# Performance work log

Measured on AMD Instinct MI355X. Metric: run time of the kernel, lower is better.

Reference implementation:

```python
import jax, jax.numpy as jnp
import numpy as np

EPS = 1e-6
NUM_HEADS = 16

def rmsnorm(x, w):
    # x: [..., d], w: [d]
    norm = jax.lax.rsqrt(jnp.mean(x * x, axis=-1, keepdims=True) + EPS)
    return w * (x * norm)

def setup_inputs() -> dict:
    key = jax.random.key(0)
    ks = jax.random.split(key, 6)
    B, N, C = 2, 2048, 1024
    H = NUM_HEADS
    hd = C // H
    x = jax.random.normal(ks[0], (B, N, C), dtype=jnp.float32)
    scale = 1.0 / np.sqrt(C)
    qkv_w = jax.random.normal(ks[1], (C, 3 * C), dtype=jnp.float32) * scale
    qkv_b = jnp.zeros((3 * C,), dtype=jnp.float32)
    q_norm_w = jnp.ones((hd,), dtype=jnp.float32)
    k_norm_w = jnp.ones((hd,), dtype=jnp.float32)
    proj_w = jax.random.normal(ks[2], (C, C), dtype=jnp.float32) * scale
    proj_b = jnp.zeros((C,), dtype=jnp.float32)
    return {"x": x, "qkv_w": qkv_w, "qkv_b": qkv_b,
            "q_norm_w": q_norm_w, "k_norm_w": k_norm_w,
            "proj_w": proj_w, "proj_b": proj_b}

def reference(x, qkv_w, qkv_b, q_norm_w, k_norm_w, proj_w, proj_b):
    B, N, C = x.shape
    H = NUM_HEADS
    hd = C // H
    qkv = x @ qkv_w + qkv_b                       # [B,N,3C]
    qkv = qkv.reshape(B, N, 3, H, hd)
    q, k, v = qkv[:, :, 0], qkv[:, :, 1], qkv[:, :, 2]  # [B,N,H,hd]
    q = jnp.transpose(q, (0, 2, 1, 3))            # [B,H,N,hd]
    k = jnp.transpose(k, (0, 2, 1, 3))
    v = jnp.transpose(v, (0, 2, 1, 3))
    q = rmsnorm(q, q_norm_w)
    k = rmsnorm(k, k_norm_w)
    scores = jnp.einsum('bhqd,bhkd->bhqk', q, k) / jnp.sqrt(jnp.float32(hd))
    attn = jax.nn.softmax(scores, axis=-1)
    out = jnp.einsum('bhqk,bhkd->bhqd', attn, v)  # [B,H,N,hd]
    out = jnp.transpose(out, (0, 2, 1, 3)).reshape(B, N, C)
    return out @ proj_w + proj_b
```

## Files before the change

kernel.cpp:

```cpp
#include <hip/hip_runtime.h>

typedef unsigned short u16;
typedef unsigned int u32;
typedef __bf16 bf16x8 __attribute__((ext_vector_type(8)));
typedef float f32x4 __attribute__((ext_vector_type(4)));
typedef unsigned short u16x8 __attribute__((ext_vector_type(8)));
typedef unsigned short u16x4 __attribute__((ext_vector_type(4)));

__device__ __forceinline__ float bf2f(u16 u) {
    union { unsigned int i; float f; } c; c.i = ((unsigned int)u) << 16; return c.f;
}
__device__ __forceinline__ u16 f2bf(float f) {
    union { float f; unsigned int i; } c; c.f = f;
    unsigned int r = c.i + 0x7FFFu + ((c.i >> 16) & 1u);
    return (u16)(r >> 16);
}
__device__ __forceinline__ u16 f2bf_rtz(float f) {
    union { float f; unsigned int i; } c; c.f = f;
    return (u16)(c.i >> 16);
}
__device__ __forceinline__ float fast_exp2(float x) {
#if __has_builtin(__builtin_amdgcn_exp2f)
    return __builtin_amdgcn_exp2f(x);
#else
    return exp2f(x);
#endif
}
__device__ __forceinline__ bf16x8 u2b(u16x8 v) {
    return __builtin_bit_cast(bf16x8, v);
}
__device__ __forceinline__ void async16(const void* g, void* l) {
    __builtin_amdgcn_global_load_lds(
        (const __attribute__((address_space(1))) u32*)g,
        (__attribute__((address_space(3))) u32*)l, 16, 0, 0);
}

__global__ __launch_bounds__(256) void prep(
    const float* __restrict__ X, u16* __restrict__ Xb,
    const float* __restrict__ qkv_w, u16* __restrict__ qwT,
    const float* __restrict__ proj_w, u16* __restrict__ pwT)
{
    __shared__ float tile[32][33];
    const int blk = blockIdx.x;
    const int t = threadIdx.x;
    if (blk < 2048) {
        const size_t i = ((size_t)blk * 256 + t) * 8;
        u16x8 h;
        #pragma unroll
        for (int e = 0; e < 8; ++e) h[e] = f2bf(X[i + e]);
        *(u16x8*)&Xb[i] = h;
        return;
    }
    const float* W; u16* Th; int K, N, bx, by;
    if (blk < 5120) {
        W = qkv_w; Th = qwT; K = 1024; N = 3072;
        bx = (blk - 2048) % 96; by = (blk - 2048) / 96;
    } else {
        W = proj_w; Th = pwT; K = 1024; N = 1024;
        bx = (blk - 5120) % 32; by = (blk - 5120) / 32;
    }
    const int bk = by * 32, bn = bx * 32;
    const int tx = t & 31, ty = t >> 5;
    #pragma unroll
    for (int r = ty; r < 32; r += 8)
        tile[r][tx] = W[(size_t)(bk + r) * N + bn + tx];
    __syncthreads();
    #pragma unroll
    for (int r = ty; r < 32; r += 8)
        Th[(size_t)(bn + r) * K + bk + tx] = f2bf(tile[tx][r]);
}

__global__ __launch_bounds__(256) void gemm_qkv(
    const u16* __restrict__ AH, const u16* __restrict__ BH,
    const float* __restrict__ bias,
    u16* __restrict__ Qb, u16* __restrict__ Kb, u16* __restrict__ Vt,
    const float* __restrict__ qw, const float* __restrict__ kw)
{
    const int K = 1024;
    __shared__ __align__(16) u16 AhT[128 * 32];
    __shared__ __align__(16) u16 BhT[128 * 32];
    const int t = threadIdx.x;
    const int bm = blockIdx.y * 128, bn = blockIdx.x * 128;
    const int wave = t >> 6, lane = t & 63;
    const int wm = (wave >> 1) * 64, wn = (wave & 1) * 64;
    const int l15 = lane & 15, quad = lane >> 4;
    const int srow = lane >> 2, scol = (lane & 3) * 8;

    f32x4 acc[4][4];
    const f32x4 zero = {0.0f, 0.0f, 0.0f, 0.0f};
    #pragma unroll
    for (int i = 0; i < 4; ++i)
        #pragma unroll
        for (int j = 0; j < 4; ++j) acc[i][j] = zero;

    for (int k0 = 0; k0 < K; k0 += 32) {
        #pragma unroll
        for (int rr = 0; rr < 2; ++rr) {
            const int r0 = (rr * 4 + wave) * 16;
            const size_t ga = (size_t)(bm + r0 + srow) * K + k0 + scol;
            const size_t gb = (size_t)(bn + r0 + srow) * K + k0 + scol;
            async16(&AH[ga], &AhT[r0 * 32]);
            async16(&BH[gb], &BhT[r0 * 32]);
        }
        __syncthreads();
        bf16x8 ah[4], bh[4];
        #pragma unroll
        for (int i = 0; i < 4; ++i)
            ah[i] = *(const bf16x8*)&AhT[(wm + i * 16 + l15) * 32 + quad * 8];
        #pragma unroll
        for (int j = 0; j < 4; ++j)
            bh[j] = *(const bf16x8*)&BhT[(wn + j * 16 + l15) * 32 + quad * 8];
        #pragma unroll
        for (int i = 0; i < 4; ++i)
            #pragma unroll
            for (int j = 0; j < 4; ++j)
                acc[i][j] = __builtin_amdgcn_mfma_f32_16x16x32_bf16(
                    ah[i], bh[j], acc[i][j], 0, 0, 0);
        __syncthreads();
    }

    const int gc0 = bn + wn;
    const int sec = gc0 >> 10;
    const int h = (gc0 & 1023) >> 6;
    const int b = bm >> 11;
    const int bhd = b * 16 + h;
    float bv[4], wj[4];
    #pragma unroll
    for (int j = 0; j < 4; ++j) {
        const int d = j * 16 + l15;
        bv[j] = bias[gc0 + d];
        wj[j] = (sec == 2) ? 0.0f : (sec ? kw[d] : qw[d] * 0.18033688011f);
    }
    if (sec < 2) {
        u16* dst = sec ? Kb : Qb;
        #pragma unroll
        for (int i = 0; i < 4; ++i) {
            float val[4][4];
            float ss[4] = {0.0f, 0.0f, 0.0f, 0.0f};
            #pragma unroll
            for (int j = 0; j < 4; ++j)
                #pragma unroll
                for (int r = 0; r < 4; ++r) {
                    val[j][r] = acc[i][j][r] + bv[j];
                    ss[r] += val[j][r] * val[j][r];
                }
            #pragma unroll
            for (int r = 0; r < 4; ++r) {
                #pragma unroll
                for (int m = 1; m < 16; m <<= 1)
                    ss[r] += __shfl_xor(ss[r], m, 64);
                const float nrm = rsqrtf(ss[r] * 0.015625f + 1e-6f);
                const int n = (bm + wm + i * 16 + quad * 4 + r) & 2047;
                const size_t rowb = ((size_t)bhd * 2048 + n) * 64;
                #pragma unroll
                for (int j = 0; j < 4; ++j)
                    dst[rowb + j * 16 + l15] = f2bf(val[j][r] * nrm * wj[j]);
            }
        }
    } else {
        const int nb = (bm + wm) & 2047;
        #pragma unroll
        for (int i = 0; i < 4; ++i) {
            const int s0 = (i & 1) * 32 + quad * 8 + (i >> 1) * 4;
            #pragma unroll
            for (int j = 0; j < 4; ++j) {
                const int d = j * 16 + l15;
                u16x4 pk;
                #pragma unroll
                for (int r = 0; r < 4; ++r)
                    pk[r] = f2bf(acc[i][j][r] + bv[j]);
                *(u16x4*)&Vt[((size_t)bhd * 64 + d) * 2048 + nb + s0] = pk;
            }
        }
    }
}

__global__ __launch_bounds__(256) void gemm_proj(
    const u16* __restrict__ AH, const u16* __restrict__ BH,
    const float* __restrict__ bias, float* __restrict__ C)
{
    const int N = 1024, K = 1024;
    __shared__ __align__(16) u16 AhT[64 * 32];
    __shared__ __align__(16) u16 BhT[128 * 32];
    const int t = threadIdx.x;
    const int bm = blockIdx.y * 64, bn = blockIdx.x * 128;
    const int wave = t >> 6, lane = t & 63;
    const int l15 = lane & 15, quad = lane >> 4;
    const int srow = lane >> 2, scol = (lane & 3) * 8;

    f32x4 acc[4][2];
    const f32x4 zero = {0.0f, 0.0f, 0.0f, 0.0f};
    #pragma unroll
    for (int i = 0; i < 4; ++i)
        #pragma unroll
        for (int j = 0; j < 2; ++j) acc[i][j] = zero;

    for (int k0 = 0; k0 < K; k0 += 32) {
        {
            const int r0 = wave * 16;
            async16(&AH[(size_t)(bm + r0 + srow) * K + k0 + scol],
                    &AhT[r0 * 32]);
        }
        #pragma unroll
        for (int cc = 0; cc < 2; ++cc) {
            const int r0 = (wave * 2 + cc) * 16;
            async16(&BH[(size_t)(bn + r0 + srow) * K + k0 + scol],
                    &BhT[r0 * 32]);
        }
        __syncthreads();
        bf16x8 ah[4], bh[2];
        #pragma unroll
        for (int i = 0; i < 4; ++i)
            ah[i] = *(const bf16x8*)&AhT[(i * 16 + l15) * 32 + quad * 8];
        #pragma unroll
        for (int j = 0; j < 2; ++j)
            bh[j] = *(const bf16x8*)
                &BhT[(wave * 32 + j * 16 + l15) * 32 + quad * 8];
        #pragma unroll
        for (int i = 0; i < 4; ++i)
            #pragma unroll
            for (int j = 0; j < 2; ++j)
                acc[i][j] = __builtin_amdgcn_mfma_f32_16x16x32_bf16(
                    ah[i], bh[j], acc[i][j], 0, 0, 0);
        __syncthreads();
    }

    #pragma unroll
    for (int j = 0; j < 2; ++j) {
        const int col = bn + wave * 32 + j * 16 + l15;
        const float bv = bias[col];
        #pragma unroll
        for (int i = 0; i < 4; ++i) {
            const int row = bm + i * 16 + quad * 4;
            #pragma unroll
            for (int r = 0; r < 4; ++r)
                C[(size_t)(row + r) * N + col] = acc[i][j][r] + bv;
        }
    }
}

__global__ __launch_bounds__(128) void flash_attn_mfma(
    const u16* __restrict__ Qb, const u16* __restrict__ Kb,
    const u16* __restrict__ Vt, u16* __restrict__ Attn)
{
    __shared__ __align__(16) u16 Klds[2 * 64 * 64];
    __shared__ __align__(16) u16 Vlds[2 * 64 * 64];

    const int t = threadIdx.x;
    const int bid = blockIdx.x;
    const int bh = bid & 31;
    const int qt = bid >> 5;
    const int n0 = qt * 64;
    const size_t kbase = (size_t)bh * 2048 * 64;
    const size_t vbase = (size_t)bh * 64 * 2048;
    const int wave = t >> 6, lane = t & 63;
    const int l15 = lane & 15, quad = lane >> 4;
    const int srow8 = lane >> 3;
    const int sgrp = lane & 7;

    bf16x8 qf[2][2];
    #pragma unroll
    for (int qs = 0; qs < 2; ++qs) {
        const size_t qrow =
            ((size_t)bh * 2048 + n0 + wave * 32 + qs * 16 + l15) * 64;
        qf[qs][0] = *(const bf16x8*)&Qb[qrow + quad * 8];
        qf[qs][1] = *(const bf16x8*)&Qb[qrow + 32 + quad * 8];
    }

    int kofs[4][2];
    #pragma unroll
    for (int nt = 0; nt < 4; ++nt) {
        const int row = nt * 16 + l15;
        kofs[nt][0] = row * 64 + ((quad ^ (row & 7)) * 8);
        kofs[nt][1] = row * 64 + (((quad + 4) ^ (row & 7)) * 8);
    }

    f32x4 o[2][4];
    const f32x4 zero = {0.0f, 0.0f, 0.0f, 0.0f};
    #pragma unroll
    for (int qs = 0; qs < 2; ++qs)
        #pragma unroll
        for (int dt = 0; dt < 4; ++dt) o[qs][dt] = zero;
    f32x4 osum[2] = {zero, zero};
    bf16x8 ones;
    #pragma unroll
    for (int e = 0; e < 8; ++e) ones[e] = (__bf16)1.0f;

    #pragma unroll
    for (int cc = 0; cc < 4; ++cc) {
        const int r0 = (wave * 4 + cc) * 8;
        const int row = r0 + srow8;
        const int gg = sgrp ^ (row & 7);
        async16(&Kb[kbase + (size_t)row * 64 + gg * 8], &Klds[r0 * 64]);
        async16(&Vt[vbase + (size_t)row * 2048 + gg * 8], &Vlds[r0 * 64]);
    }

    for (int kt = 0; kt < 32; ++kt) {
        __syncthreads();
        if (kt + 1 < 32) {
            const int nb = ((kt + 1) & 1) * 4096;
            #pragma unroll
            for (int cc = 0; cc < 4; ++cc) {
                const int r0 = (wave * 4 + cc) * 8;
                const int row = r0 + srow8;
                const int gg = sgrp ^ (row & 7);
                async16(&Kb[kbase + (size_t)((kt + 1) * 64 + row) * 64 + gg * 8],
                        &Klds[nb + r0 * 64]);
                async16(&Vt[vbase + (size_t)row * 2048 + (kt + 1) * 64 + gg * 8],
                        &Vlds[nb + r0 * 64]);
            }
        }
        const int cb = (kt & 1) * 4096;

        f32x4 s[2][4];
        #pragma unroll
        for (int nt = 0; nt < 4; ++nt) {
            bf16x8 kf0 = *(const bf16x8*)&Klds[cb + kofs[nt][0]];
            bf16x8 kf1 = *(const bf16x8*)&Klds[cb + kofs[nt][1]];
            __builtin_amdgcn_s_setprio(1);
            #pragma unroll
            for (int qs = 0; qs < 2; ++qs) {
                s[qs][nt] = __builtin_amdgcn_mfma_f32_16x16x32_bf16(
                    kf0, qf[qs][0], zero, 0, 0, 0);
                s[qs][nt] = __builtin_amdgcn_mfma_f32_16x16x32_bf16(
                    kf1, qf[qs][1], s[qs][nt], 0, 0, 0);
            }
            __builtin_amdgcn_s_setprio(0);
        }

        bf16x8 pf[2][2];
        #pragma unroll
        for (int qs = 0; qs < 2; ++qs) {
            #pragma unroll
            for (int m = 0; m < 2; ++m) {
                u16x8 pk;
                #pragma unroll
                for (int r = 0; r < 4; ++r) {
                    pk[r]     = f2bf_rtz(fast_exp2(s[qs][m][r]));
                    pk[4 + r] = f2bf_rtz(fast_exp2(s[qs][m + 2][r]));
                }
                pf[qs][m] = u2b(pk);
            }
        }

        #pragma unroll
        for (int dt = 0; dt < 4; ++dt) {
            bf16x8 vf0 = *(const bf16x8*)&Vlds[cb + kofs[dt][0]];
            bf16x8 vf1 = *(const bf16x8*)&Vlds[cb + kofs[dt][1]];
            __builtin_amdgcn_s_setprio(1);
            #pragma unroll
            for (int qs = 0; qs < 2; ++qs) {
                o[qs][dt] = __builtin_amdgcn_mfma_f32_16x16x32_bf16(
                    pf[qs][0], vf0, o[qs][dt], 0, 0, 0);
                o[qs][dt] = __builtin_amdgcn_mfma_f32_16x16x32_bf16(
                    pf[qs][1], vf1, o[qs][dt], 0, 0, 0);
            }
            __builtin_amdgcn_s_setprio(0);
        }
        __builtin_amdgcn_s_setprio(1);
        #pragma unroll
        for (int qs = 0; qs < 2; ++qs) {
            osum[qs] = __builtin_amdgcn_mfma_f32_16x16x32_bf16(
                pf[qs][0], ones, osum[qs], 0, 0, 0);
            osum[qs] = __builtin_amdgcn_mfma_f32_16x16x32_bf16(
                pf[qs][1], ones, osum[qs], 0, 0, 0);
        }
        __builtin_amdgcn_s_setprio(0);
    }

    const size_t obase =
        ((size_t)(bh >> 4) * 2048 + n0) * 1024 + (bh & 15) * 64;
    #pragma unroll
    for (int qs = 0; qs < 2; ++qs)
        #pragma unroll
        for (int r = 0; r < 4; ++r) {
            const float inv = 1.0f / osum[qs][r];
            const size_t rbase =
                obase + (size_t)(wave * 32 + qs * 16 + quad * 4 + r) * 1024;
            #pragma unroll
            for (int dt = 0; dt < 4; ++dt)
                Attn[rbase + dt * 16 + l15] = f2bf(o[qs][dt][r] * inv);
        }
}

extern "C" void kernel_launch(void* const* d_in, const int* in_sizes, int n_in,
                              void* d_out, int out_size, void* d_ws, size_t ws_size,
                              hipStream_t stream)
{
    const float* x      = (const float*)d_in[0];
    const float* qkv_w  = (const float*)d_in[1];
    const float* qkv_b  = (const float*)d_in[2];
    const float* q_nw   = (const float*)d_in[3];
    const float* k_nw   = (const float*)d_in[4];
    const float* proj_w = (const float*)d_in[5];
    const float* proj_b = (const float*)d_in[6];
    float* out = (float*)d_out;

    char* ws = (char*)d_ws;
    u16* AttnB = (u16*)ws;
    u16* qwT   = (u16*)(ws + 8388608);
    u16* pwT   = (u16*)(ws + 14680064);
    u16* Xb    = (u16*)(ws + 16777216);
    u16* QbB   = (u16*)(ws + 25165824);
    u16* KbB   = (u16*)(ws + 33554432);
    u16* VtB   = (u16*)(ws + 41943040);
    (void)in_sizes; (void)n_in; (void)out_size;
    if (ws_size < 50331648u) return;

    prep<<<dim3(6144), 256, 0, stream>>>(x, Xb, qkv_w, qwT, proj_w, pwT);
    gemm_qkv<<<dim3(3072 / 128, 4096 / 128), 256, 0, stream>>>(
        Xb, qwT, qkv_b, QbB, KbB, VtB, q_nw, k_nw);
    flash_attn_mfma<<<dim3(1024), 128, 0, stream>>>(QbB, KbB, VtB, AttnB);
    gemm_proj<<<dim3(1024 / 128, 4096 / 64), 256, 0, stream>>>(
        AttnB, pwT, proj_b, out);
}
```

Before: 199.7 us.

## Double-buffer GEMM LDS tiles and enlarge flash-attention query and key tiles

Both GEMM kernels now keep two LDS buffers and prefetch the next K-slice asynchronously while the current one feeds the MFMAs. This drops one barrier per iteration and is meant to hide global load latency behind compute. The attention kernel moves to 256 threads with 128 queries per block, and each loop stage stages 128 keys as two 64-key halves. That halves the per-query K/V traffic and the number of loop barriers, at the cost of twice the LDS per block and half as many blocks.

```diff
diff --git a/kernel.cpp b/kernel.cpp
--- a/kernel.cpp
+++ b/kernel.cpp
@@ -77,8 +77,8 @@
     const float* __restrict__ qw, const float* __restrict__ kw)
 {
     const int K = 1024;
-    __shared__ __align__(16) u16 AhT[128 * 32];
-    __shared__ __align__(16) u16 BhT[128 * 32];
+    __shared__ __align__(16) u16 AhT[2 * 128 * 32];
+    __shared__ __align__(16) u16 BhT[2 * 128 * 32];
     const int t = threadIdx.x;
     const int bm = blockIdx.y * 128, bn = blockIdx.x * 128;
     const int wave = t >> 6, lane = t & 63;
@@ -93,30 +93,42 @@
         #pragma unroll
         for (int j = 0; j < 4; ++j) acc[i][j] = zero;
 
+    #pragma unroll
+    for (int rr = 0; rr < 2; ++rr) {
+        const int r0 = (rr * 4 + wave) * 16;
+        async16(&AH[(size_t)(bm + r0 + srow) * K + scol], &AhT[r0 * 32]);
+        async16(&BH[(size_t)(bn + r0 + srow) * K + scol], &BhT[r0 * 32]);
+    }
+
+    int cur = 0;
     for (int k0 = 0; k0 < K; k0 += 32) {
-        #pragma unroll
-        for (int rr = 0; rr < 2; ++rr) {
-            const int r0 = (rr * 4 + wave) * 16;
-            const size_t ga = (size_t)(bm + r0 + srow) * K + k0 + scol;
-            const size_t gb = (size_t)(bn + r0 + srow) * K + k0 + scol;
-            async16(&AH[ga], &AhT[r0 * 32]);
-            async16(&BH[gb], &BhT[r0 * 32]);
-        }
         __syncthreads();
+        if (k0 + 32 < K) {
+            const int nb = (cur ^ 1) * 4096;
+            #pragma unroll
+            for (int rr = 0; rr < 2; ++rr) {
+                const int r0 = (rr * 4 + wave) * 16;
+                async16(&AH[(size_t)(bm + r0 + srow) * K + k0 + 32 + scol],
+                        &AhT[nb + r0 * 32]);
+                async16(&BH[(size_t)(bn + r0 + srow) * K + k0 + 32 + scol],
+                        &BhT[nb + r0 * 32]);
+            }
+        }
+        const int cb = cur * 4096;
         bf16x8 ah[4], bh[4];
         #pragma unroll
         for (int i = 0; i < 4; ++i)
-            ah[i] = *(const bf16x8*)&AhT[(wm + i * 16 + l15) * 32 + quad * 8];
+            ah[i] = *(const bf16x8*)&AhT[cb + (wm + i * 16 + l15) * 32 + quad * 8];
         #pragma unroll
         for (int j = 0; j < 4; ++j)
-            bh[j] = *(const bf16x8*)&BhT[(wn + j * 16 + l15) * 32 + quad * 8];
+            bh[j] = *(const bf16x8*)&BhT[cb + (wn + j * 16 + l15) * 32 + quad * 8];
         #pragma unroll
         for (int i = 0; i < 4; ++i)
             #pragma unroll
             for (int j = 0; j < 4; ++j)
                 acc[i][j] = __builtin_amdgcn_mfma_f32_16x16x32_bf16(
                     ah[i], bh[j], acc[i][j], 0, 0, 0);
-        __syncthreads();
+        cur ^= 1;
     }
 
     const int gc0 = bn + wn;
@@ -180,8 +192,8 @@
     const float* __restrict__ bias, float* __restrict__ C)
 {
     const int N = 1024, K = 1024;
-    __shared__ __align__(16) u16 AhT[64 * 32];
-    __shared__ __align__(16) u16 BhT[128 * 32];
+    __shared__ __align__(16) u16 AhT[2 * 64 * 32];
+    __shared__ __align__(16) u16 BhT[2 * 128 * 32];
     const int t = threadIdx.x;
     const int bm = blockIdx.y * 64, bn = blockIdx.x * 128;
     const int wave = t >> 6, lane = t & 63;
@@ -195,34 +207,49 @@
         #pragma unroll
         for (int j = 0; j < 2; ++j) acc[i][j] = zero;
 
+    {
+        const int r0 = wave * 16;
+        async16(&AH[(size_t)(bm + r0 + srow) * K + scol], &AhT[r0 * 32]);
+    }
+    #pragma unroll
+    for (int cc = 0; cc < 2; ++cc) {
+        const int r0 = (wave * 2 + cc) * 16;
+        async16(&BH[(size_t)(bn + r0 + srow) * K + scol], &BhT[r0 * 32]);
+    }
+
+    int cur = 0;
     for (int k0 = 0; k0 < K; k0 += 32) {
-        {
-            const int r0 = wave * 16;
-            async16(&AH[(size_t)(bm + r0 + srow) * K + k0 + scol],
-                    &AhT[r0 * 32]);
-        }
-        #pragma unroll
-        for (int cc = 0; cc < 2; ++cc) {
-            const int r0 = (wave * 2 + cc) * 16;
-            async16(&BH[(size_t)(bn + r0 + srow) * K + k0 + scol],
-                    &BhT[r0 * 32]);
-        }
         __syncthreads();
+        if (k0 + 32 < K) {
+            const int nbA = (cur ^ 1) * 2048, nbB = (cur ^ 1) * 4096;
+            {
+                const int r0 = wave * 16;
+                async16(&AH[(size_t)(bm + r0 + srow) * K + k0 + 32 + scol],
+                        &AhT[nbA + r0 * 32]);
+            }
+            #pragma unroll
+            for (int cc = 0; cc < 2; ++cc) {
+                const int r0 = (wave * 2 + cc) * 16;
+                async16(&BH[(size_t)(bn + r0 + srow) * K + k0 + 32 + scol],
+                        &BhT[nbB + r0 * 32]);
+            }
+        }
+        const int cbA = cur * 2048, cbB = cur * 4096;
         bf16x8 ah[4], bh[2];
         #pragma unroll
         for (int i = 0; i < 4; ++i)
-            ah[i] = *(const bf16x8*)&AhT[(i * 16 + l15) * 32 + quad * 8];
+            ah[i] = *(const bf16x8*)&AhT[cbA + (i * 16 + l15) * 32 + quad * 8];
         #pragma unroll
         for (int j = 0; j < 2; ++j)
             bh[j] = *(const bf16x8*)
-                &BhT[(wave * 32 + j * 16 + l15) * 32 + quad * 8];
+                &BhT[cbB + (wave * 32 + j * 16 + l15) * 32 + quad * 8];
         #pragma unroll
         for (int i = 0; i < 4; ++i)
             #pragma unroll
             for (int j = 0; j < 2; ++j)
                 acc[i][j] = __builtin_amdgcn_mfma_f32_16x16x32_bf16(
                     ah[i], bh[j], acc[i][j], 0, 0, 0);
-        __syncthreads();
+        cur ^= 1;
     }
 
     #pragma unroll
@@ -239,18 +266,18 @@
     }
 }
 
-__global__ __launch_bounds__(128) void flash_attn_mfma(
+__global__ __launch_bounds__(256) void flash_attn_mfma(
     const u16* __restrict__ Qb, const u16* __restrict__ Kb,
     const u16* __restrict__ Vt, u16* __restrict__ Attn)
 {
-    __shared__ __align__(16) u16 Klds[2 * 64 * 64];
-    __shared__ __align__(16) u16 Vlds[2 * 64 * 64];
+    __shared__ __align__(16) u16 Klds[2 * 2 * 64 * 64];
+    __shared__ __align__(16) u16 Vlds[2 * 2 * 64 * 64];
 
     const int t = threadIdx.x;
     const int bid = blockIdx.x;
     const int bh = bid & 31;
     const int qt = bid >> 5;
-    const int n0 = qt * 64;
+    const int n0 = qt * 128;
     const size_t kbase = (size_t)bh * 2048 * 64;
     const size_t vbase = (size_t)bh * 64 * 2048;
     const int wave = t >> 6, lane = t & 63;
@@ -287,85 +314,99 @@
     for (int e = 0; e < 8; ++e) ones[e] = (__bf16)1.0f;
 
     #pragma unroll
-    for (int cc = 0; cc < 4; ++cc) {
-        const int r0 = (wave * 4 + cc) * 8;
-        const int row = r0 + srow8;
-        const int gg = sgrp ^ (row & 7);
-        async16(&Kb[kbase + (size_t)row * 64 + gg * 8], &Klds[r0 * 64]);
-        async16(&Vt[vbase + (size_t)row * 2048 + gg * 8], &Vlds[r0 * 64]);
-    }
-
-    for (int kt = 0; kt < 32; ++kt) {
+    for (int h = 0; h < 2; ++h)
+        #pragma unroll
+        for (int cc = 0; cc < 2; ++cc) {
+            const int r0 = (wave + cc * 4) * 8;
+            const int row = r0 + srow8;
+            const int gg = sgrp ^ (row & 7);
+            async16(&Kb[kbase + (size_t)(h * 64 + row) * 64 + gg * 8],
+                    &Klds[h * 4096 + r0 * 64]);
+            async16(&Vt[vbase + (size_t)row * 2048 + h * 64 + gg * 8],
+                    &Vlds[h * 4096 + r0 * 64]);
+        }
+
+    for (int kt = 0; kt < 16; ++kt) {
         __syncthreads();
-        if (kt + 1 < 32) {
-            const int nb = ((kt + 1) & 1) * 4096;
-            #pragma unroll
-            for (int cc = 0; cc < 4; ++cc) {
-                const int r0 = (wave * 4 + cc) * 8;
-                const int row = r0 + srow8;
-                const int gg = sgrp ^ (row & 7);
-                async16(&Kb[kbase + (size_t)((kt + 1) * 64 + row) * 64 + gg * 8],
-                        &Klds[nb + r0 * 64]);
-                async16(&Vt[vbase + (size_t)row * 2048 + (kt + 1) * 64 + gg * 8],
-                        &Vlds[nb + r0 * 64]);
-            }
-        }
-        const int cb = (kt & 1) * 4096;
-
-        f32x4 s[2][4];
-        #pragma unroll
-        for (int nt = 0; nt < 4; ++nt) {
-            bf16x8 kf0 = *(const bf16x8*)&Klds[cb + kofs[nt][0]];
-            bf16x8 kf1 = *(const bf16x8*)&Klds[cb + kofs[nt][1]];
+        if (kt + 1 < 16) {
+            const int nb = ((kt + 1) & 1) * 8192;
+            #pragma unroll
+            for (int h = 0; h < 2; ++h)
+                #pragma unroll
+                for (int cc = 0; cc < 2; ++cc) {
+                    const int r0 = (wave + cc * 4) * 8;
+                    const int row = r0 + srow8;
+                    const int gg = sgrp ^ (row & 7);
+                    async16(&Kb[kbase +
+                                (size_t)((kt + 1) * 128 + h * 64 + row) * 64 +
+                                gg * 8],
+                            &Klds[nb + h * 4096 + r0 * 64]);
+                    async16(&Vt[vbase + (size_t)row * 2048 +
+                                (kt + 1) * 128 + h * 64 + gg * 8],
+                            &Vlds[nb + h * 4096 + r0 * 64]);
+                }
+        }
+        const int cb = (kt & 1) * 8192;
+
+        #pragma unroll
+        for (int h = 0; h < 2; ++h) {
+            const int hb = cb + h * 4096;
+
+            f32x4 s[2][4];
+            #pragma unroll
+            for (int nt = 0; nt < 4; ++nt) {
+                bf16x8 kf0 = *(const bf16x8*)&Klds[hb + kofs[nt][0]];
+                bf16x8 kf1 = *(const bf16x8*)&Klds[hb + kofs[nt][1]];
+                __builtin_amdgcn_s_setprio(1);
+                #pragma unroll
+                for (int qs = 0; qs < 2; ++qs) {
+                    s[qs][nt] = __builtin_amdgcn_mfma_f32_16x16x32_bf16(
+                        kf0, qf[qs][0], zero, 0, 0, 0);
+                    s[qs][nt] = __builtin_amdgcn_mfma_f32_16x16x32_bf16(
+                        kf1, qf[qs][1], s[qs][nt], 0, 0, 0);
+                }
+                __builtin_amdgcn_s_setprio(0);
+            }
+
+            bf16x8 pf[2][2];
+            #pragma unroll
+            for (int qs = 0; qs < 2; ++qs) {
+                #pragma unroll
+                for (int m = 0; m < 2; ++m) {
+                    u16x8 pk;
+                    #pragma unroll
+                    for (int r = 0; r < 4; ++r) {
+                        pk[r]     = f2bf_rtz(fast_exp2(s[qs][m][r]));
+                        pk[4 + r] = f2bf_rtz(fast_exp2(s[qs][m + 2][r]));
+                    }
+                    pf[qs][m] = u2b(pk);
+                }
+            }
+
+            #pragma unroll
+            for (int dt = 0; dt < 4; ++dt) {
+                bf16x8 vf0 = *(const bf16x8*)&Vlds[hb + kofs[dt][0]];
+                bf16x8 vf1 = *(const bf16x8*)&Vlds[hb + kofs[dt][1]];
+                __builtin_amdgcn_s_setprio(1);
+                #pragma unroll
+                for (int qs = 0; qs < 2; ++qs) {
+                    o[qs][dt] = __builtin_amdgcn_mfma_f32_16x16x32_bf16(
+                        pf[qs][0], vf0, o[qs][dt], 0, 0, 0);
+                    o[qs][dt] = __builtin_amdgcn_mfma_f32_16x16x32_bf16(
+                        pf[qs][1], vf1, o[qs][dt], 0, 0, 0);
+                }
+                __builtin_amdgcn_s_setprio(0);
+            }
             __builtin_amdgcn_s_setprio(1);
             #pragma unroll
             for (int qs = 0; qs < 2; ++qs) {
-                s[qs][nt] = __builtin_amdgcn_mfma_f32_16x16x32_bf16(
-                    kf0, qf[qs][0], zero, 0, 0, 0);
-                s[qs][nt] = __builtin_amdgcn_mfma_f32_16x16x32_bf16(
-                    kf1, qf[qs][1], s[qs][nt], 0, 0, 0);
+                osum[qs] = __builtin_amdgcn_mfma_f32_16x16x32_bf16(
+                    pf[qs][0], ones, osum[qs], 0, 0, 0);
+                osum[qs] = __builtin_amdgcn_mfma_f32_16x16x32_bf16(
+                    pf[qs][1], ones, osum[qs], 0, 0, 0);
             }
             __builtin_amdgcn_s_setprio(0);
         }
-
-        bf16x8 pf[2][2];
-        #pragma unroll
-        for (int qs = 0; qs < 2; ++qs) {
-            #pragma unroll
-            for (int m = 0; m < 2; ++m) {
-                u16x8 pk;
-                #pragma unroll
-                for (int r = 0; r < 4; ++r) {
-                    pk[r]     = f2bf_rtz(fast_exp2(s[qs][m][r]));
-                    pk[4 + r] = f2bf_rtz(fast_exp2(s[qs][m + 2][r]));
-                }
-                pf[qs][m] = u2b(pk);
-            }
-        }
-
-        #pragma unroll
-        for (int dt = 0; dt < 4; ++dt) {
-            bf16x8 vf0 = *(const bf16x8*)&Vlds[cb + kofs[dt][0]];
-            bf16x8 vf1 = *(const bf16x8*)&Vlds[cb + kofs[dt][1]];
-            __builtin_amdgcn_s_setprio(1);
-            #pragma unroll
-            for (int qs = 0; qs < 2; ++qs) {
-                o[qs][dt] = __builtin_amdgcn_mfma_f32_16x16x32_bf16(
-                    pf[qs][0], vf0, o[qs][dt], 0, 0, 0);
-                o[qs][dt] = __builtin_amdgcn_mfma_f32_16x16x32_bf16(
-                    pf[qs][1], vf1, o[qs][dt], 0, 0, 0);
-            }
-            __builtin_amdgcn_s_setprio(0);
-        }
-        __builtin_amdgcn_s_setprio(1);
-        #pragma unroll
-        for (int qs = 0; qs < 2; ++qs) {
-            osum[qs] = __builtin_amdgcn_mfma_f32_16x16x32_bf16(
-                pf[qs][0], ones, osum[qs], 0, 0, 0);
-            osum[qs] = __builtin_amdgcn_mfma_f32_16x16x32_bf16(
-                pf[qs][1], ones, osum[qs], 0, 0, 0);
-        }
-        __builtin_amdgcn_s_setprio(0);
     }
 
     const size_t obase =
@@ -410,7 +451,7 @@
     prep<<<dim3(6144), 256, 0, stream>>>(x, Xb, qkv_w, qwT, proj_w, pwT);
     gemm_qkv<<<dim3(3072 / 128, 4096 / 128), 256, 0, stream>>>(
         Xb, qwT, qkv_b, QbB, KbB, VtB, q_nw, k_nw);
-    flash_attn_mfma<<<dim3(1024), 128, 0, stream>>>(QbB, KbB, VtB, AttnB);
+    flash_attn_mfma<<<dim3(512), 256, 0, stream>>>(QbB, KbB, VtB, AttnB);
     gemm_proj<<<dim3(1024 / 128, 4096 / 64), 256, 0, stream>>>(
         AttnB, pwT, proj_b, out);
 }
```

After: 203.8 us. 2.1% more time.
